# Performance work log

Measured on AMD Instinct MI355X. Metric: run time of the kernel, lower is better.

Reference implementation:

```python
import jax, jax.numpy as jnp
import numpy as np

C = 64          # channels
K = 15          # sum(shell_sizes)=1+14
H = 32          # neighbors per query
N = 50000       # support points (== query points M)
RADIUS = 1.0
SIGMA = 0.7
INF = 1e6
BN_EPS = 1e-5


def _init_kernel_points(key):
    # stand-in for load_kernels: 1 center point + 14 points on a sphere shell
    pts = jax.random.normal(key, (K - 1, 3), dtype=jnp.float32)
    pts = pts / jnp.linalg.norm(pts, axis=1, keepdims=True) * RADIUS
    return jnp.concatenate([jnp.zeros((1, 3), jnp.float32), pts], axis=0)


def setup_inputs() -> dict:
    key = jax.random.key(0)
    ks = jax.random.split(key, 10)
    q_pts = jax.random.normal(ks[0], (N, 3), dtype=jnp.float32)
    s_pts = jax.random.normal(ks[1], (N, 3), dtype=jnp.float32)
    s_feats = jax.random.normal(ks[2], (N, C), dtype=jnp.float32)
    neighb_inds = jax.random.randint(ks[3], (N, H), 0, N)
    kernel_points = _init_kernel_points(ks[4])
    # alpha_mlp: Linear(C->C, no bias) -> BatchNorm -> LeakyReLU(0.1) -> Linear(C->K*C)
    lim1 = 1.0 / np.sqrt(C)
    W1 = jax.random.uniform(ks[5], (C, C), jnp.float32, -lim1, lim1)
    gamma = jnp.ones((C,), jnp.float32)
    beta = jnp.zeros((C,), jnp.float32)
    W2 = jax.random.uniform(ks[6], (C, K * C), jnp.float32, -lim1, lim1)
    b2 = jax.random.uniform(ks[7], (K * C,), jnp.float32, -lim1, lim1)
    return {"q_pts": q_pts, "s_pts": s_pts, "s_feats": s_feats,
            "neighb_inds": neighb_inds, "kernel_points": kernel_points,
            "W1": W1, "gamma": gamma, "beta": beta, "W2": W2, "b2": b2}


def reference(q_pts, s_pts, s_feats, neighb_inds, kernel_points, W1, gamma, beta, W2, b2):
    M = q_pts.shape[0]
    # alpha_mlp on pooled (= center) features: (M, C) -> (M, K*C)
    h = s_feats @ W1
    mu = jnp.mean(h, axis=0)
    var = jnp.var(h, axis=0)
    h = (h - mu) / jnp.sqrt(var + BN_EPS) * gamma + beta
    h = jax.nn.leaky_relu(h, 0.1)
    conv_weights = (h @ W2 + b2).reshape(M, K, C)

    # gather neighbor features with a zero padding row (index N -> zeros)
    padded_feats = jnp.concatenate([s_feats, jnp.zeros((1, C), s_feats.dtype)], axis=0)
    neighbor_feats = padded_feats[neighb_inds]                 # (M, H, C)

    # relative neighbor positions with inf padding point
    s_pts_pad = jnp.concatenate([s_pts, jnp.full((1, 3), INF, s_pts.dtype)], axis=0)
    neighbors = s_pts_pad[neighb_inds] - q_pts[:, None, :]     # (M, H, 3)

    # kernel-point influence: nearest kernel point + linear influence
    diff = neighbors[:, :, None, :] - kernel_points            # (M, H, K, 3)
    sq_d = jnp.sum(diff * diff, axis=-1)                       # (M, H, K)
    nn_sq = jnp.min(sq_d, axis=-1)                             # (M, H)
    nn_idx = jnp.argmin(sq_d, axis=-1)                         # (M, H)
    infl = jnp.clip(1.0 - jnp.sqrt(nn_sq) / SIGMA, 0.0)        # (M, H)

    # per-neighbor channel weights from the MLP output, gathered by 1nn kernel point
    nw = jnp.take_along_axis(conv_weights, nn_idx[:, :, None], axis=1)  # (M, H, C)
    nw = nw * infl[:, :, None]

    # weighted aggregation (merge=mul, aggr=sum over neighbors)
    return jnp.sum(neighbor_feats * nw, axis=1)                # (M, C)
```

## Files before the change

kernel.cpp:

```cpp
#include <hip/hip_runtime.h>
#include <math.h>

#define N_PTS 50000
#define CCH   64
#define KP    15
#define NH    32
#define SIGMA 0.7f
#define BN_EPS 1e-5f
#define LEAKY 0.1f
#define QB    16
#define CWS   18
#define STATS_BLOCKS 512

typedef short bf16x8 __attribute__((ext_vector_type(8)));
typedef float floatx4 __attribute__((ext_vector_type(4)));

__device__ __forceinline__ unsigned short f2b(float f) {
    union { float f; unsigned u; } v; v.f = f;
    return (unsigned short)((v.u + 0x7FFFu + ((v.u >> 16) & 1u)) >> 16);
}
__device__ __forceinline__ float b2f(unsigned short b) {
    union { unsigned u; float f; } v; v.u = ((unsigned)b) << 16;
    return v.f;
}

__global__ __launch_bounds__(256) void k_prep(const float* __restrict__ sf,
                                              const float* __restrict__ W1,
                                              const float* __restrict__ W2,
                                              float* __restrict__ bn,
                                              unsigned short* __restrict__ hst,
                                              unsigned short* __restrict__ w2b) {
    int t = threadIdx.x;
    if (blockIdx.x >= STATS_BLOCKS) {
        int g = (blockIdx.x - STATS_BLOCKS) * 256 + t;
        int lane = g & 63, s = (g >> 6) & 1, tt = g >> 7;
        int col = lane & 15, quad = lane >> 4;
        int base = (s * 32 + quad * 8) * 960 + tt * 16 + col;
        ushort4 lo, hi;
        lo.x = f2b(W2[base + 0 * 960]); lo.y = f2b(W2[base + 1 * 960]);
        lo.z = f2b(W2[base + 2 * 960]); lo.w = f2b(W2[base + 3 * 960]);
        hi.x = f2b(W2[base + 4 * 960]); hi.y = f2b(W2[base + 5 * 960]);
        hi.z = f2b(W2[base + 6 * 960]); hi.w = f2b(W2[base + 7 * 960]);
        *(ushort4*)(w2b + g * 8)     = lo;
        *(ushort4*)(w2b + g * 8 + 4) = hi;
        return;
    }
    int c = t & 63, ml = t >> 6;
    float w1c[64];
    #pragma unroll
    for (int i = 0; i < 64; ++i) w1c[i] = W1[i * 64 + c];
    __shared__ float rows[4][64];
    float acc_s = 0.f, acc_q = 0.f;
    for (int m0 = blockIdx.x * 4; m0 < N_PTS; m0 += STATS_BLOCKS * 4) {
        __syncthreads();
        ((float*)rows)[t] = sf[m0 * 64 + t];
        __syncthreads();
        float h = 0.f;
        #pragma unroll
        for (int i4 = 0; i4 < 16; ++i4) {
            float4 r = *(const float4*)&rows[ml][i4 * 4];
            h += r.x * w1c[i4 * 4] + r.y * w1c[i4 * 4 + 1]
               + r.z * w1c[i4 * 4 + 2] + r.w * w1c[i4 * 4 + 3];
        }
        acc_s += h;
        acc_q += h * h;
        hst[(m0 + ml) * 64 + c] = f2b(h);
    }
    __shared__ float red[2][256];
    red[0][t] = acc_s; red[1][t] = acc_q;
    __syncthreads();
    if (t < 64) {
        float s = red[0][t] + red[0][64 + t] + red[0][128 + t] + red[0][192 + t];
        float q = red[1][t] + red[1][64 + t] + red[1][128 + t] + red[1][192 + t];
        atomicAdd(&bn[t], s);
        atomicAdd(&bn[64 + t], q);
    }
}

__global__ __launch_bounds__(256, 4) void k_main(
    const float* __restrict__ q_pts, const float* __restrict__ s_pts,
    const float* __restrict__ s_feats, const int* __restrict__ nb,
    const float* __restrict__ kpts, const float* __restrict__ gamma,
    const float* __restrict__ beta, const float* __restrict__ bn,
    const float* __restrict__ b2, const unsigned short* __restrict__ w2b,
    const unsigned short* __restrict__ hst, float* __restrict__ out) {

    __shared__ __align__(16) unsigned short cwT[960 * CWS];
    __shared__ float abS[128];
    __shared__ float kp[48];
    __shared__ int   nCnt[QB];
    __shared__ int   nPack[QB][NH];
    __shared__ float nInf[QB][NH];

    int t = threadIdx.x;
    int lane = t & 63, wv = t >> 6;
    int m0 = blockIdx.x * QB;

    if (t < 64) {
        float mu  = bn[t] * (1.0f / N_PTS);
        float var = bn[64 + t] * (1.0f / N_PTS) - mu * mu;
        float a   = gamma[t] * rsqrtf(var + BN_EPS);
        abS[t]      = a;
        abS[64 + t] = beta[t] - mu * a;
    }
    if (t < KP * 3) kp[t] = kpts[t];
    if (t >= 240) nCnt[t - 240] = 0;
    __syncthreads();

    int row = lane & 15, half = lane >> 4;
    bf16x8 a0, a1;
    {
        const unsigned short* hrow = hst + (m0 + row) * 64 + half * 8;
        bf16x8 r0 = *(const bf16x8*)(hrow);
        bf16x8 r1 = *(const bf16x8*)(hrow + 32);
        #pragma unroll
        for (int j = 0; j < 8; ++j) {
            int c0 = half * 8 + j;
            float g0 = abS[c0] * b2f((unsigned short)r0[j]) + abS[64 + c0];
            g0 = g0 > 0.f ? g0 : LEAKY * g0;
            a0[j] = (short)f2b(g0);
            int c1 = 32 + half * 8 + j;
            float g1 = abS[c1] * b2f((unsigned short)r1[j]) + abS[64 + c1];
            g1 = g1 > 0.f ? g1 : LEAKY * g1;
            a1[j] = (short)f2b(g1);
        }
    }

    {
        int col = lane & 15, quad = lane >> 4;
        for (int ti = 0; ti < 15; ++ti) {
            int tt = wv * 15 + ti;
            bf16x8 bf0 = *(const bf16x8*)(w2b + ((tt * 2 + 0) * 64 + lane) * 8);
            bf16x8 bf1 = *(const bf16x8*)(w2b + ((tt * 2 + 1) * 64 + lane) * 8);
            floatx4 acc = {0.f, 0.f, 0.f, 0.f};
            acc = __builtin_amdgcn_mfma_f32_16x16x32_bf16(a0, bf0, acc, 0, 0, 0);
            acc = __builtin_amdgcn_mfma_f32_16x16x32_bf16(a1, bf1, acc, 0, 0, 0);
            int n = tt * 16 + col;
            float bb = b2[n];
            unsigned short* dst = &cwT[n * CWS + quad * 4];
            ushort2 w01, w23;
            w01.x = f2b(acc[0] + bb); w01.y = f2b(acc[1] + bb);
            w23.x = f2b(acc[2] + bb); w23.y = f2b(acc[3] + bb);
            *(ushort2*)(dst)     = w01;
            *(ushort2*)(dst + 2) = w23;
        }
    }

    for (int task = t; task < QB * NH; task += 256) {
        int q = task >> 5, hh = task & 31;
        int m = m0 + q;
        int idx = nb[m * NH + hh];
        float px = s_pts[idx * 3 + 0] - q_pts[m * 3 + 0];
        float py = s_pts[idx * 3 + 1] - q_pts[m * 3 + 1];
        float pz = s_pts[idx * 3 + 2] - q_pts[m * 3 + 2];
        float best = 1e30f; int bi = 0;
        #pragma unroll
        for (int k = 0; k < KP; ++k) {
            float dx = px - kp[k * 3], dy = py - kp[k * 3 + 1], dz = pz - kp[k * 3 + 2];
            float d = dx * dx + dy * dy + dz * dz;
            if (d < best) { best = d; bi = k; }
        }
        float infl = 1.f - sqrtf(best) * (1.0f / SIGMA);
        if (infl > 0.f) {
            int pos = atomicAdd(&nCnt[q], 1);
            nPack[q][pos] = idx | (bi << 20);
            nInf[q][pos]  = infl;
        }
    }
    __syncthreads();

    {
        int c = lane;
        #pragma unroll
        for (int qi = 0; qi < 4; ++qi) {
            int q = wv * 4 + qi;
            int na = nCnt[q];
            float acc = 0.f;
            int jj = 0;
            for (; jj + 1 < na; jj += 2) {
                int p0 = nPack[q][jj], p1 = nPack[q][jj + 1];
                float i0 = nInf[q][jj], i1 = nInf[q][jj + 1];
                float f0 = s_feats[(p0 & 0xFFFFF) * 64 + c];
                float f1 = s_feats[(p1 & 0xFFFFF) * 64 + c];
                float w0 = b2f(cwT[((p0 >> 20) * 64 + c) * CWS + q]);
                float w1 = b2f(cwT[((p1 >> 20) * 64 + c) * CWS + q]);
                acc += i0 * f0 * w0 + i1 * f1 * w1;
            }
            if (jj < na) {
                int p0 = nPack[q][jj];
                float f0 = s_feats[(p0 & 0xFFFFF) * 64 + c];
                float w0 = b2f(cwT[((p0 >> 20) * 64 + c) * CWS + q]);
                acc += nInf[q][jj] * f0 * w0;
            }
            out[(m0 + q) * 64 + c] = acc;
        }
    }
}

extern "C" void kernel_launch(void* const* d_in, const int* in_sizes, int n_in,
                              void* d_out, int out_size, void* d_ws, size_t ws_size,
                              hipStream_t stream) {
    const float* q_pts   = (const float*)d_in[0];
    const float* s_pts   = (const float*)d_in[1];
    const float* s_feats = (const float*)d_in[2];
    const int*   nb      = (const int*)d_in[3];
    const float* kpts    = (const float*)d_in[4];
    const float* W1      = (const float*)d_in[5];
    const float* gamma   = (const float*)d_in[6];
    const float* beta    = (const float*)d_in[7];
    const float* W2      = (const float*)d_in[8];
    const float* b2      = (const float*)d_in[9];
    float* out = (float*)d_out;

    float* ws = (float*)d_ws;
    float* bn = ws;
    unsigned short* w2b = (unsigned short*)(ws + 128);
    unsigned short* hst = w2b + 61440;

    hipMemsetAsync(bn, 0, 128 * sizeof(float), stream);
    k_prep<<<STATS_BLOCKS + 30, 256, 0, stream>>>(s_feats, W1, W2, bn, hst, w2b);
    k_main<<<N_PTS / QB, 256, 0, stream>>>(q_pts, s_pts, s_feats, nb, kpts,
                                           gamma, beta, bn, b2, w2b, hst, out);
}
```

Before: 161.8 us.

## Use 1024-thread blocks with one wave per query and overlapped neighbor scan

The main kernel now launches 1024 threads per block, where it used 256. The 512 neighbor tasks run in parallel with the MFMA weight-tile generation before a single barrier, the 60 tiles are spread across 16 waves, and each wave aggregates exactly one query with a 4-way unrolled loop. The stats pass in the prep kernel also doubles its block count. The aim is to raise occupancy within the LDS limit and cut serial per-wave work. The cost is tighter register limits from the new launch bounds and larger per-block barriers.

Result: slower. 242.0 us (+49.6%).

```diff
diff --git a/kernel.cpp b/kernel.cpp
--- a/kernel.cpp
+++ b/kernel.cpp
@@ -10,7 +10,7 @@
 #define LEAKY 0.1f
 #define QB    16
 #define CWS   18
-#define STATS_BLOCKS 512
+#define STATS_BLOCKS 1024
 
 typedef short bf16x8 __attribute__((ext_vector_type(8)));
 typedef float floatx4 __attribute__((ext_vector_type(4)));
@@ -77,7 +77,7 @@
     }
 }
 
-__global__ __launch_bounds__(256, 4) void k_main(
+__global__ __launch_bounds__(1024, 8) void k_main(
     const float* __restrict__ q_pts, const float* __restrict__ s_pts,
     const float* __restrict__ s_feats, const int* __restrict__ nb,
     const float* __restrict__ kpts, const float* __restrict__ gamma,
@@ -102,9 +102,11 @@
         float a   = gamma[t] * rsqrtf(var + BN_EPS);
         abS[t]      = a;
         abS[64 + t] = beta[t] - mu * a;
-    }
-    if (t < KP * 3) kp[t] = kpts[t];
-    if (t >= 240) nCnt[t - 240] = 0;
+    } else if (t < 64 + 45) {
+        kp[t - 64] = kpts[t - 64];
+    } else if (t >= 128 && t < 128 + QB) {
+        nCnt[t - 128] = 0;
+    }
     __syncthreads();
 
     int row = lane & 15, half = lane >> 4;
@@ -119,17 +121,38 @@
             float g0 = abS[c0] * b2f((unsigned short)r0[j]) + abS[64 + c0];
             g0 = g0 > 0.f ? g0 : LEAKY * g0;
             a0[j] = (short)f2b(g0);
-            int c1 = 32 + half * 8 + j;
+            int c1 = 32 + c0;
             float g1 = abS[c1] * b2f((unsigned short)r1[j]) + abS[64 + c1];
             g1 = g1 > 0.f ? g1 : LEAKY * g1;
             a1[j] = (short)f2b(g1);
         }
     }
 
+    if (t < QB * NH) {
+        int q = t >> 5, hh = t & 31;
+        int m = m0 + q;
+        int idx = nb[m * NH + hh];
+        float px = s_pts[idx * 3 + 0] - q_pts[m * 3 + 0];
+        float py = s_pts[idx * 3 + 1] - q_pts[m * 3 + 1];
+        float pz = s_pts[idx * 3 + 2] - q_pts[m * 3 + 2];
+        float best = 1e30f; int bi = 0;
+        #pragma unroll
+        for (int k = 0; k < KP; ++k) {
+            float dx = px - kp[k * 3], dy = py - kp[k * 3 + 1], dz = pz - kp[k * 3 + 2];
+            float d = dx * dx + dy * dy + dz * dz;
+            if (d < best) { best = d; bi = k; }
+        }
+        float infl = 1.f - sqrtf(best) * (1.0f / SIGMA);
+        if (infl > 0.f) {
+            int pos = atomicAdd(&nCnt[q], 1);
+            nPack[q][pos] = idx | (bi << 20);
+            nInf[q][pos]  = infl;
+        }
+    }
+
     {
         int col = lane & 15, quad = lane >> 4;
-        for (int ti = 0; ti < 15; ++ti) {
-            int tt = wv * 15 + ti;
+        for (int tt = wv; tt < 60; tt += 16) {
             bf16x8 bf0 = *(const bf16x8*)(w2b + ((tt * 2 + 0) * 64 + lane) * 8);
             bf16x8 bf1 = *(const bf16x8*)(w2b + ((tt * 2 + 1) * 64 + lane) * 8);
             floatx4 acc = {0.f, 0.f, 0.f, 0.f};
@@ -145,55 +168,39 @@
             *(ushort2*)(dst + 2) = w23;
         }
     }
-
-    for (int task = t; task < QB * NH; task += 256) {
-        int q = task >> 5, hh = task & 31;
-        int m = m0 + q;
-        int idx = nb[m * NH + hh];
-        float px = s_pts[idx * 3 + 0] - q_pts[m * 3 + 0];
-        float py = s_pts[idx * 3 + 1] - q_pts[m * 3 + 1];
-        float pz = s_pts[idx * 3 + 2] - q_pts[m * 3 + 2];
-        float best = 1e30f; int bi = 0;
-        #pragma unroll
-        for (int k = 0; k < KP; ++k) {
-            float dx = px - kp[k * 3], dy = py - kp[k * 3 + 1], dz = pz - kp[k * 3 + 2];
-            float d = dx * dx + dy * dy + dz * dz;
-            if (d < best) { best = d; bi = k; }
-        }
-        float infl = 1.f - sqrtf(best) * (1.0f / SIGMA);
-        if (infl > 0.f) {
-            int pos = atomicAdd(&nCnt[q], 1);
-            nPack[q][pos] = idx | (bi << 20);
-            nInf[q][pos]  = infl;
-        }
-    }
     __syncthreads();
 
     {
+        int q = wv;
         int c = lane;
-        #pragma unroll
-        for (int qi = 0; qi < 4; ++qi) {
-            int q = wv * 4 + qi;
-            int na = nCnt[q];
-            float acc = 0.f;
-            int jj = 0;
-            for (; jj + 1 < na; jj += 2) {
-                int p0 = nPack[q][jj], p1 = nPack[q][jj + 1];
-                float i0 = nInf[q][jj], i1 = nInf[q][jj + 1];
-                float f0 = s_feats[(p0 & 0xFFFFF) * 64 + c];
-                float f1 = s_feats[(p1 & 0xFFFFF) * 64 + c];
-                float w0 = b2f(cwT[((p0 >> 20) * 64 + c) * CWS + q]);
-                float w1 = b2f(cwT[((p1 >> 20) * 64 + c) * CWS + q]);
-                acc += i0 * f0 * w0 + i1 * f1 * w1;
-            }
-            if (jj < na) {
-                int p0 = nPack[q][jj];
-                float f0 = s_feats[(p0 & 0xFFFFF) * 64 + c];
-                float w0 = b2f(cwT[((p0 >> 20) * 64 + c) * CWS + q]);
-                acc += nInf[q][jj] * f0 * w0;
-            }
-            out[(m0 + q) * 64 + c] = acc;
-        }
+        int na = nCnt[q];
+        float acc = 0.f;
+        int jj = 0;
+        for (; jj + 4 <= na; jj += 4) {
+            int   p0 = nPack[q][jj + 0], p1 = nPack[q][jj + 1];
+            int   p2 = nPack[q][jj + 2], p3 = nPack[q][jj + 3];
+            float i0 = nInf[q][jj + 0], i1 = nInf[q][jj + 1];
+            float i2 = nInf[q][jj + 2], i3 = nInf[q][jj + 3];
+            float f0 = s_feats[(p0 & 0xFFFFF) * 64 + c];
+            float f1 = s_feats[(p1 & 0xFFFFF) * 64 + c];
+            float f2 = s_feats[(p2 & 0xFFFFF) * 64 + c];
+            float f3 = s_feats[(p3 & 0xFFFFF) * 64 + c];
+            float w0 = b2f(cwT[((p0 >> 20) * 64 + c) * CWS + q]);
+            float w1 = b2f(cwT[((p1 >> 20) * 64 + c) * CWS + q]);
+            float w2 = b2f(cwT[((p2 >> 20) * 64 + c) * CWS + q]);
+            float w3 = b2f(cwT[((p3 >> 20) * 64 + c) * CWS + q]);
+            acc += i0 * f0 * w0;
+            acc += i1 * f1 * w1;
+            acc += i2 * f2 * w2;
+            acc += i3 * f3 * w3;
+        }
+        for (; jj < na; ++jj) {
+            int p0 = nPack[q][jj];
+            float f0 = s_feats[(p0 & 0xFFFFF) * 64 + c];
+            float w0 = b2f(cwT[((p0 >> 20) * 64 + c) * CWS + q]);
+            acc += nInf[q][jj] * f0 * w0;
+        }
+        out[(m0 + q) * 64 + c] = acc;
     }
 }
 
@@ -219,6 +226,6 @@
 
     hipMemsetAsync(bn, 0, 128 * sizeof(float), stream);
     k_prep<<<STATS_BLOCKS + 30, 256, 0, stream>>>(s_feats, W1, W2, bn, hst, w2b);
-    k_main<<<N_PTS / QB, 256, 0, stream>>>(q_pts, s_pts, s_feats, nb, kpts,
-                                           gamma, beta, bn, b2, w2b, hst, out);
-}
+    k_main<<<N_PTS / QB, 1024, 0, stream>>>(q_pts, s_pts, s_feats, nb, kpts,
+                                            gamma, beta, bn, b2, w2b, hst, out);
+}
```
